# Kernel optimization log

Hardware: AMD Instinct MI355X
Metric: run time of the kernel (lower is better)

The kernel has to match this reference:

```python
import jax, jax.numpy as jnp
import numpy as np

KH, KW = 3, 3
STRIDE = (1, 1)
PAD = 1


def _patches(x):
    # x: (B, C, H, W) -> (B, C, KH, KW, OH, OW)
    B, C, H, W = x.shape
    p = jax.lax.conv_general_dilated_patches(
        x, filter_shape=(KH, KW), window_strides=STRIDE,
        padding=[(PAD, PAD), (PAD, PAD)],
        dimension_numbers=('NCHW', 'OIHW', 'NCHW'))
    OH, OW = p.shape[2], p.shape[3]
    # feature dim of patches is ordered (C, KH, KW) — channel-major
    return p.reshape(B, C, KH, KW, OH, OW)


def setup_inputs() -> dict:
    key = jax.random.key(0)
    k1, k2 = jax.random.split(key, 2)
    B, C, H, W, O = 8, 32, 64, 64, 32
    OH = (H - KH + 2 * PAD) // STRIDE[0] + 1
    OW = (W - KW + 2 * PAD) // STRIDE[1] + 1
    x = jax.random.normal(k1, (B, C, H, W), dtype=jnp.float32)
    # xavier_uniform on the 6D weight (torch fan-in/out convention):
    recf = O * C * KH * KW
    fan_in, fan_out = OW * recf, OH * recf
    limit = float(np.sqrt(6.0 / (fan_in + fan_out)))
    weights = jax.random.uniform(k2, (OH, OW, O, C, KH, KW),
                                 minval=-limit, maxval=limit,
                                 dtype=jnp.float32)
    bias = jnp.zeros((O,), dtype=jnp.float32)
    return {"x": x, "weights": weights, "bias": bias}


def reference(x, weights, bias):
    # locally connected 2D conv: unique weight per output location.
    p = _patches(x)  # (B, C, KH, KW, OH, OW)
    # Faithful to the torch einsum 'bchw,ocwh->bo': the weight's kernel
    # spatial dims (kH,kW) are labeled (w,h), i.e. spatially transposed
    # relative to the patch.
    out = jnp.einsum('bchwij,ijocwh->boij', p, weights)
    return out + bias[None, :, None, None]
```

## Files before the change

kernel.cpp:

```cpp
#include <hip/hip_runtime.h>
#include <hip/hip_bf16.h>


#define NB 8
#define NC 32
#define NO 32
#define NH 64
#define NW 64
#define KK 288
#define LOCS 4
#define XCOLS 6
#define BSTRIDE 578
#define XNAT_SZ (NB * BSTRIDE)

typedef __attribute__((ext_vector_type(8))) short s16x8;
typedef __attribute__((ext_vector_type(4))) float f32x4;

union Frag { unsigned short s[8]; uint4 q; s16x8 v; };

__device__ __forceinline__ unsigned short f2bf(float f) {
  __hip_bfloat16 h = __float2bfloat16(f);
  return *reinterpret_cast<unsigned short*>(&h);
}

__global__ __launch_bounds__(512) void lc2d_kernel(
    const float* __restrict__ x, const float* __restrict__ w,
    const float* __restrict__ bias, float* __restrict__ out) {
  const int bid = blockIdx.x;
  const int g = (bid & 7) * 128 + (bid >> 3);
  const int loc0 = g * LOCS;
  const int i = loc0 >> 6;
  const int j0 = loc0 & 63;
  const int t = threadIdx.x;
  const int lane = t & 63;
  const int wv = t >> 6;
  const int m16 = lane & 15;
  const int kg = lane >> 4;
  const int l = wv >> 1;
  const int ot = wv & 1;
  const int bm = m16 & 7;

  __shared__ float xnat[XNAT_SZ];
  __shared__ float obuf[LOCS][NB][NO];

  float sv[9];
#pragma unroll
  for (int it = 0; it < 9; ++it) {
    int e = t + it * 512;
    int b_ = e / 576;
    int r = e - b_ * 576;
    int row = r / XCOLS;
    int cc = r - row * XCOLS;
    int c = row / 3;
    int yy = row - c * 3;
    int y = i + yy - 1;
    int xc = j0 + cc - 1;
    float v = 0.f;
    if ((unsigned)y < 64u && (unsigned)xc < 64u)
      v = x[((b_ * NC + c) * NH + y) * NW + xc];
    sv[it] = v;
  }
  asm volatile("" ::: "memory");

  float4 wf[18];
  {
    const float* wp =
        w + ((size_t)(loc0 + l) * NO + ot * 16 + m16) * KK + kg * 8;
#pragma unroll
    for (int ks = 0; ks < 9; ++ks) {
      wf[2 * ks]     = *(const float4*)(wp + ks * 32);
      wf[2 * ks + 1] = *(const float4*)(wp + ks * 32 + 4);
    }
  }

#pragma unroll
  for (int it = 0; it < 9; ++it) {
    int e = t + it * 512;
    int b_ = e / 576;
    int r = e - b_ * 576;
    xnat[b_ * BSTRIDE + r] = sv[it];
  }
  asm volatile("s_waitcnt lgkmcnt(0)\n\ts_barrier" ::: "memory");

  uint4 afr[9];
#pragma unroll
  for (int ks = 0; ks < 9; ++ks) {
    Frag f;
#pragma unroll
    for (int e = 0; e < 8; ++e) {
      int k = ks * 32 + kg * 8 + e;
      int c = k / 9;
      int rem = k - c * 9;
      int a = rem / 3;
      int bb = rem - a * 3;
      f.s[e] = f2bf(xnat[bm * BSTRIDE + (c * 3 + bb) * XCOLS + l + a]);
    }
    afr[ks] = f.q;
  }

  f32x4 acc = {0.f, 0.f, 0.f, 0.f};
#pragma unroll
  for (int ks = 0; ks < 9; ++ks) {
    float4 lo = wf[2 * ks], hi = wf[2 * ks + 1];
    Frag fb;
    fb.s[0] = f2bf(lo.x); fb.s[1] = f2bf(lo.y);
    fb.s[2] = f2bf(lo.z); fb.s[3] = f2bf(lo.w);
    fb.s[4] = f2bf(hi.x); fb.s[5] = f2bf(hi.y);
    fb.s[6] = f2bf(hi.z); fb.s[7] = f2bf(hi.w);
    Frag fa; fa.q = afr[ks];
    acc = __builtin_amdgcn_mfma_f32_16x16x32_bf16(fa.v, fb.v, acc, 0, 0, 0);
  }

  if (kg < 2) {
#pragma unroll
    for (int r = 0; r < 4; ++r)
      obuf[l][kg * 4 + r][ot * 16 + m16] = acc[r];
  }
  asm volatile("s_waitcnt lgkmcnt(0)\n\ts_barrier" ::: "memory");

  if (t < 256) {
    const int b_ = t >> 5;
    const int o_ = t & 31;
    const float bia = bias[o_];
    float4 r4;
    r4.x = obuf[0][b_][o_] + bia;
    r4.y = obuf[1][b_][o_] + bia;
    r4.z = obuf[2][b_][o_] + bia;
    r4.w = obuf[3][b_][o_] + bia;
    *reinterpret_cast<float4*>(
        &out[((size_t)(b_ * NO + o_) * NH + i) * NW + j0]) = r4;
  }
}

extern "C" void kernel_launch(void* const* d_in, const int* in_sizes, int n_in,
                              void* d_out, int out_size, void* d_ws, size_t ws_size,
                              hipStream_t stream) {
  const float* x    = (const float*)d_in[0];
  const float* w    = (const float*)d_in[1];
  const float* bias = (const float*)d_in[2];
  float* out = (float*)d_out;
  lc2d_kernel<<<dim3(NH * NW / LOCS), dim3(512), 0, stream>>>(x, w, bias, out);
}
```

Baseline: 37.06 us.

## Use one output location per block with coalesced weight staging through LDS

Each block now handles a single output location with 128 threads instead of four locations with 512 threads, launching four times as many blocks. The whole 32x288 weight slab is loaded with fully contiguous float4 reads and staged in padded LDS, replacing the per-lane strided global weight loads. The output is written directly from the MFMA accumulators, which drops the obuf staging buffer and the second barrier. In exchange there are more blocks with more LDS each, and the output stores become scattered scalar writes instead of float4 writes.

```diff
diff --git a/kernel.cpp b/kernel.cpp
--- a/kernel.cpp
+++ b/kernel.cpp
@@ -8,10 +8,8 @@
 #define NH 64
 #define NW 64
 #define KK 288
-#define LOCS 4
-#define XCOLS 6
-#define BSTRIDE 578
-#define XNAT_SZ (NB * BSTRIDE)
+#define WS4 73
+#define XBS 292
 
 typedef __attribute__((ext_vector_type(8))) short s16x8;
 typedef __attribute__((ext_vector_type(4))) float f32x4;
@@ -23,62 +21,61 @@
   return *reinterpret_cast<unsigned short*>(&h);
 }
 
-__global__ __launch_bounds__(512) void lc2d_kernel(
+__global__ __launch_bounds__(128, 2) void lc2d_kernel(
     const float* __restrict__ x, const float* __restrict__ w,
     const float* __restrict__ bias, float* __restrict__ out) {
   const int bid = blockIdx.x;
-  const int g = (bid & 7) * 128 + (bid >> 3);
-  const int loc0 = g * LOCS;
-  const int i = loc0 >> 6;
-  const int j0 = loc0 & 63;
+  const int g = (bid & 7) * 512 + (bid >> 3);
+  const int i = g >> 6;
+  const int j0 = g & 63;
   const int t = threadIdx.x;
   const int lane = t & 63;
-  const int wv = t >> 6;
+  const int ot = t >> 6;
   const int m16 = lane & 15;
   const int kg = lane >> 4;
-  const int l = wv >> 1;
-  const int ot = wv & 1;
   const int bm = m16 & 7;
+  const int o_ = ot * 16 + m16;
 
-  __shared__ float xnat[XNAT_SZ];
-  __shared__ float obuf[LOCS][NB][NO];
+  __shared__ float4 ws4[NO * WS4];
+  __shared__ float xnat[NB * XBS];
 
-  float sv[9];
+  float xv_[18];
 #pragma unroll
-  for (int it = 0; it < 9; ++it) {
-    int e = t + it * 512;
-    int b_ = e / 576;
-    int r = e - b_ * 576;
-    int row = r / XCOLS;
-    int cc = r - row * XCOLS;
-    int c = row / 3;
-    int yy = row - c * 3;
-    int y = i + yy - 1;
-    int xc = j0 + cc - 1;
+  for (int it = 0; it < 18; ++it) {
+    int e = t + it * 128;
+    int row = e / 3;
+    int a = e - row * 3;
+    int b_ = row / 96;
+    int rem = row - b_ * 96;
+    int c = rem / 3;
+    int bb = rem - c * 3;
+    int y = i + bb - 1;
+    int xc = j0 + a - 1;
     float v = 0.f;
     if ((unsigned)y < 64u && (unsigned)xc < 64u)
       v = x[((b_ * NC + c) * NH + y) * NW + xc];
-    sv[it] = v;
-  }
-  asm volatile("" ::: "memory");
-
-  float4 wf[18];
-  {
-    const float* wp =
-        w + ((size_t)(loc0 + l) * NO + ot * 16 + m16) * KK + kg * 8;
-#pragma unroll
-    for (int ks = 0; ks < 9; ++ks) {
-      wf[2 * ks]     = *(const float4*)(wp + ks * 32);
-      wf[2 * ks + 1] = *(const float4*)(wp + ks * 32 + 4);
-    }
+    xv_[it] = v;
   }
 
+  const float4* wb = reinterpret_cast<const float4*>(w + (size_t)g * NO * KK);
+  float4 wv_[18];
 #pragma unroll
-  for (int it = 0; it < 9; ++it) {
-    int e = t + it * 512;
-    int b_ = e / 576;
-    int r = e - b_ * 576;
-    xnat[b_ * BSTRIDE + r] = sv[it];
+  for (int it = 0; it < 18; ++it) wv_[it] = wb[t + it * 128];
+
+  const float bia = bias[o_];
+
+#pragma unroll
+  for (int it = 0; it < 18; ++it) {
+    int e = t + it * 128;
+    int b_ = e / 288;
+    xnat[e + 4 * b_] = xv_[it];
+  }
+#pragma unroll
+  for (int it = 0; it < 18; ++it) {
+    int f = t + it * 128;
+    int o = f / 72;
+    int r = f - o * 72;
+    ws4[o * WS4 + r] = wv_[it];
   }
   asm volatile("s_waitcnt lgkmcnt(0)\n\ts_barrier" ::: "memory");
 
@@ -93,7 +90,7 @@
       int rem = k - c * 9;
       int a = rem / 3;
       int bb = rem - a * 3;
-      f.s[e] = f2bf(xnat[bm * BSTRIDE + (c * 3 + bb) * XCOLS + l + a]);
+      f.s[e] = f2bf(xnat[bm * XBS + (c * 3 + bb) * 3 + a]);
     }
     afr[ks] = f.q;
   }
@@ -101,7 +98,8 @@
   f32x4 acc = {0.f, 0.f, 0.f, 0.f};
 #pragma unroll
   for (int ks = 0; ks < 9; ++ks) {
-    float4 lo = wf[2 * ks], hi = wf[2 * ks + 1];
+    float4 lo = ws4[o_ * WS4 + ks * 8 + kg * 2];
+    float4 hi = ws4[o_ * WS4 + ks * 8 + kg * 2 + 1];
     Frag fb;
     fb.s[0] = f2bf(lo.x); fb.s[1] = f2bf(lo.y);
     fb.s[2] = f2bf(lo.z); fb.s[3] = f2bf(lo.w);
@@ -113,22 +111,10 @@
 
   if (kg < 2) {
 #pragma unroll
-    for (int r = 0; r < 4; ++r)
-      obuf[l][kg * 4 + r][ot * 16 + m16] = acc[r];
-  }
-  asm volatile("s_waitcnt lgkmcnt(0)\n\ts_barrier" ::: "memory");
-
-  if (t < 256) {
-    const int b_ = t >> 5;
-    const int o_ = t & 31;
-    const float bia = bias[o_];
-    float4 r4;
-    r4.x = obuf[0][b_][o_] + bia;
-    r4.y = obuf[1][b_][o_] + bia;
-    r4.z = obuf[2][b_][o_] + bia;
-    r4.w = obuf[3][b_][o_] + bia;
-    *reinterpret_cast<float4*>(
-        &out[((size_t)(b_ * NO + o_) * NH + i) * NW + j0]) = r4;
+    for (int r = 0; r < 4; ++r) {
+      int b_ = kg * 4 + r;
+      out[((size_t)(b_ * NO + o_) * NH + i) * NW + j0] = acc[r] + bia;
+    }
   }
 }
 
@@ -139,5 +125,5 @@
   const float* w    = (const float*)d_in[1];
   const float* bias = (const float*)d_in[2];
   float* out = (float*)d_out;
-  lc2d_kernel<<<dim3(NH * NW / LOCS), dim3(512), 0, stream>>>(x, w, bias, out);
+  lc2d_kernel<<<dim3(NH * NW), dim3(128), 0, stream>>>(x, w, bias, out);
 }
```

Measured after the change: 47.95 us. 29.4% more time.

## Halve block size and process two locations per wave with prefetched weights

Applied to the files above, without the earlier changes.

Blocks shrink from 512 to 256 threads, so each wave now computes two output locations in sequence. The second location's weights are loaded inside the first location's MFMA loop to overlap global latency with compute. This trades fewer waves per location for more work per thread and higher register pressure, and launch bounds now request 4 blocks per CU.

```diff
diff --git a/kernel.cpp b/kernel.cpp
--- a/kernel.cpp
+++ b/kernel.cpp
@@ -23,7 +23,7 @@
   return *reinterpret_cast<unsigned short*>(&h);
 }
 
-__global__ __launch_bounds__(512) void lc2d_kernel(
+__global__ __launch_bounds__(256, 4) void lc2d_kernel(
     const float* __restrict__ x, const float* __restrict__ w,
     const float* __restrict__ bias, float* __restrict__ out) {
   const int bid = blockIdx.x;
@@ -36,24 +36,26 @@
   const int wv = t >> 6;
   const int m16 = lane & 15;
   const int kg = lane >> 4;
-  const int l = wv >> 1;
+  const int bm = m16 & 7;
   const int ot = wv & 1;
-  const int bm = m16 & 7;
+  const int la = wv >> 1;
+  const int lb = la + 2;
+  const int o_ = ot * 16 + m16;
 
   __shared__ float xnat[XNAT_SZ];
   __shared__ float obuf[LOCS][NB][NO];
 
-  float sv[9];
+  float sv[18];
 #pragma unroll
-  for (int it = 0; it < 9; ++it) {
-    int e = t + it * 512;
+  for (int it = 0; it < 18; ++it) {
+    int e = t + it * 256;
     int b_ = e / 576;
     int r = e - b_ * 576;
     int row = r / XCOLS;
     int cc = r - row * XCOLS;
     int c = row / 3;
-    int yy = row - c * 3;
-    int y = i + yy - 1;
+    int bb = row - c * 3;
+    int y = i + bb - 1;
     int xc = j0 + cc - 1;
     float v = 0.f;
     if ((unsigned)y < 64u && (unsigned)xc < 64u)
@@ -65,7 +67,7 @@
   float4 wf[18];
   {
     const float* wp =
-        w + ((size_t)(loc0 + l) * NO + ot * 16 + m16) * KK + kg * 8;
+        w + ((size_t)(loc0 + la) * NO + o_) * KK + kg * 8;
 #pragma unroll
     for (int ks = 0; ks < 9; ++ks) {
       wf[2 * ks]     = *(const float4*)(wp + ks * 32);
@@ -74,61 +76,90 @@
   }
 
 #pragma unroll
-  for (int it = 0; it < 9; ++it) {
-    int e = t + it * 512;
+  for (int it = 0; it < 18; ++it) {
+    int e = t + it * 256;
     int b_ = e / 576;
     int r = e - b_ * 576;
     xnat[b_ * BSTRIDE + r] = sv[it];
   }
   asm volatile("s_waitcnt lgkmcnt(0)\n\ts_barrier" ::: "memory");
 
+  auto gather = [&](int l, uint4 afr[9]) {
+#pragma unroll
+    for (int ks = 0; ks < 9; ++ks) {
+      Frag f;
+#pragma unroll
+      for (int e = 0; e < 8; ++e) {
+        int k = ks * 32 + kg * 8 + e;
+        int c = k / 9;
+        int rem = k - c * 9;
+        int a = rem / 3;
+        int bb = rem - a * 3;
+        f.s[e] = f2bf(xnat[bm * BSTRIDE + (c * 3 + bb) * XCOLS + l + a]);
+      }
+      afr[ks] = f.q;
+    }
+  };
+
   uint4 afr[9];
+  gather(la, afr);
+  {
+    const float* wpB =
+        w + ((size_t)(loc0 + lb) * NO + o_) * KK + kg * 8;
+    f32x4 acc = {0.f, 0.f, 0.f, 0.f};
 #pragma unroll
-  for (int ks = 0; ks < 9; ++ks) {
-    Frag f;
+    for (int ks = 0; ks < 9; ++ks) {
+      float4 lo = wf[2 * ks], hi = wf[2 * ks + 1];
+      Frag fb;
+      fb.s[0] = f2bf(lo.x); fb.s[1] = f2bf(lo.y);
+      fb.s[2] = f2bf(lo.z); fb.s[3] = f2bf(lo.w);
+      fb.s[4] = f2bf(hi.x); fb.s[5] = f2bf(hi.y);
+      fb.s[6] = f2bf(hi.z); fb.s[7] = f2bf(hi.w);
+      Frag fa; fa.q = afr[ks];
+      acc = __builtin_amdgcn_mfma_f32_16x16x32_bf16(fa.v, fb.v, acc, 0, 0, 0);
+      wf[2 * ks]     = *(const float4*)(wpB + ks * 32);
+      wf[2 * ks + 1] = *(const float4*)(wpB + ks * 32 + 4);
+    }
+    if (kg < 2) {
 #pragma unroll
-    for (int e = 0; e < 8; ++e) {
-      int k = ks * 32 + kg * 8 + e;
-      int c = k / 9;
-      int rem = k - c * 9;
-      int a = rem / 3;
-      int bb = rem - a * 3;
-      f.s[e] = f2bf(xnat[bm * BSTRIDE + (c * 3 + bb) * XCOLS + l + a]);
+      for (int r = 0; r < 4; ++r)
+        obuf[la][kg * 4 + r][o_] = acc[r];
     }
-    afr[ks] = f.q;
   }
 
-  f32x4 acc = {0.f, 0.f, 0.f, 0.f};
+  gather(lb, afr);
+  {
+    f32x4 acc = {0.f, 0.f, 0.f, 0.f};
 #pragma unroll
-  for (int ks = 0; ks < 9; ++ks) {
-    float4 lo = wf[2 * ks], hi = wf[2 * ks + 1];
-    Frag fb;
-    fb.s[0] = f2bf(lo.x); fb.s[1] = f2bf(lo.y);
-    fb.s[2] = f2bf(lo.z); fb.s[3] = f2bf(lo.w);
-    fb.s[4] = f2bf(hi.x); fb.s[5] = f2bf(hi.y);
-    fb.s[6] = f2bf(hi.z); fb.s[7] = f2bf(hi.w);
-    Frag fa; fa.q = afr[ks];
-    acc = __builtin_amdgcn_mfma_f32_16x16x32_bf16(fa.v, fb.v, acc, 0, 0, 0);
-  }
-
-  if (kg < 2) {
+    for (int ks = 0; ks < 9; ++ks) {
+      float4 lo = wf[2 * ks], hi = wf[2 * ks + 1];
+      Frag fb;
+      fb.s[0] = f2bf(lo.x); fb.s[1] = f2bf(lo.y);
+      fb.s[2] = f2bf(lo.z); fb.s[3] = f2bf(lo.w);
+      fb.s[4] = f2bf(hi.x); fb.s[5] = f2bf(hi.y);
+      fb.s[6] = f2bf(hi.z); fb.s[7] = f2bf(hi.w);
+      Frag fa; fa.q = afr[ks];
+      acc = __builtin_amdgcn_mfma_f32_16x16x32_bf16(fa.v, fb.v, acc, 0, 0, 0);
+    }
+    if (kg < 2) {
 #pragma unroll
-    for (int r = 0; r < 4; ++r)
-      obuf[l][kg * 4 + r][ot * 16 + m16] = acc[r];
+      for (int r = 0; r < 4; ++r)
+        obuf[lb][kg * 4 + r][o_] = acc[r];
+    }
   }
   asm volatile("s_waitcnt lgkmcnt(0)\n\ts_barrier" ::: "memory");
 
-  if (t < 256) {
+  {
     const int b_ = t >> 5;
-    const int o_ = t & 31;
-    const float bia = bias[o_];
+    const int oo = t & 31;
+    const float bia = bias[oo];
     float4 r4;
-    r4.x = obuf[0][b_][o_] + bia;
-    r4.y = obuf[1][b_][o_] + bia;
-    r4.z = obuf[2][b_][o_] + bia;
-    r4.w = obuf[3][b_][o_] + bia;
+    r4.x = obuf[0][b_][oo] + bia;
+    r4.y = obuf[1][b_][oo] + bia;
+    r4.z = obuf[2][b_][oo] + bia;
+    r4.w = obuf[3][b_][oo] + bia;
     *reinterpret_cast<float4*>(
-        &out[((size_t)(b_ * NO + o_) * NH + i) * NW + j0]) = r4;
+        &out[((size_t)(b_ * NO + oo) * NH + i) * NW + j0]) = r4;
   }
 }
 
@@ -139,5 +170,5 @@
   const float* w    = (const float*)d_in[1];
   const float* bias = (const float*)d_in[2];
   float* out = (float*)d_out;
-  lc2d_kernel<<<dim3(NH * NW / LOCS), dim3(512), 0, stream>>>(x, w, bias, out);
+  lc2d_kernel<<<dim3(NH * NW / LOCS), dim3(256), 0, stream>>>(x, w, bias, out);
 }
```

Result: slower. 46.62 us (+25.8%).
